# Performance work log

Hardware: AMD Instinct MI355X
Metric: run time of the kernel (lower is better)

The kernel has to match this reference:

```python
import jax, jax.numpy as jnp
import numpy as np

N, E, DIN, DH, DOUT = 50000, 800000, 128, 256, 128
EPS = 1e-5
SLOPE = 0.01  # torch leaky_relu default


def setup_inputs() -> dict:
    key = jax.random.key(0)
    ks = jax.random.split(key, 8)
    w = lambda k, shape: jax.random.normal(k, shape, jnp.float32) * 0.05
    return {
        "x": jax.random.normal(ks[0], (N, DIN), jnp.float32),
        "edge_index": jax.random.randint(ks[1], (2, E), 0, N, jnp.int32),
        "W0": w(ks[2], (DH, DIN)),  "b0": jnp.zeros((DH,), jnp.float32),
        "g0": jnp.ones((DH,), jnp.float32), "be0": jnp.zeros((DH,), jnp.float32),
        "W1": w(ks[3], (DH, DH)),   "b1": jnp.zeros((DH,), jnp.float32),
        "g1": jnp.ones((DH,), jnp.float32), "be1": jnp.zeros((DH,), jnp.float32),
        "W2": w(ks[4], (DOUT, DH)), "b2": jnp.zeros((DOUT,), jnp.float32),
        "g2": jnp.ones((DOUT,), jnp.float32), "be2": jnp.zeros((DOUT,), jnp.float32),
    }


def _gcn_forward(x, edge_index, params):
    n = x.shape[0]
    loop = jnp.arange(n, dtype=edge_index.dtype)
    src = jnp.concatenate([edge_index[0], loop])  # add self-loops
    dst = jnp.concatenate([edge_index[1], loop])
    deg = jnp.zeros((n,), x.dtype).at[dst].add(1.0)
    dinv = jax.lax.rsqrt(deg)  # deg >= 1 due to self-loops
    enorm = (dinv[src] * dinv[dst])[:, None]  # [E+N, 1]

    def conv(h, W, b):
        h = h @ W.T  # linear first (PyG GCNConv), messages in out_dim
        msg = h[src] * enorm
        return jax.ops.segment_sum(msg, dst, num_segments=n) + b

    def bn(h, g, be):  # BatchNorm1d, training-mode batch stats (biased var)
        mu = h.mean(0)
        var = ((h - mu) ** 2).mean(0)
        return (h - mu) * jax.lax.rsqrt(var + EPS) * g + be

    (W0, b0, g0, be0, W1, b1, g1, be1, W2, b2, g2, be2) = params
    h = jax.nn.leaky_relu(bn(conv(x, W0, b0), g0, be0), SLOPE)
    h = jax.nn.leaky_relu(bn(conv(h, W1, b1), g1, be1), SLOPE)
    h = bn(conv(h, W2, b2), g2, be2)  # last layer: no leaky_relu
    return h


def reference(x, edge_index, W0, b0, g0, be0, W1, b1, g1, be1, W2, b2, g2, be2):
    return _gcn_forward(x, edge_index,
                        (W0, b0, g0, be0, W1, b1, g1, be1, W2, b2, g2, be2))
```

## Files before the change

### kernel.cpp

```cpp
#include <hip/hip_runtime.h>
#include <hip/hip_bf16.h>

#define N_NODES 50000
#define N_EDGES 800000
#define DIN 128
#define DH   256
#define DOUT 128
#define EPSV 1e-5f
#define SLOPE 0.01f
#define SCAN_NB ((N_NODES + 255) / 256)

typedef __bf16 bf16x8 __attribute__((ext_vector_type(8)));
typedef __bf16 bf16x4 __attribute__((ext_vector_type(4)));
typedef float  f32x4  __attribute__((ext_vector_type(4)));

__global__ void cast_kernel(const float* __restrict__ src, __bf16* __restrict__ dst, int n4) {
    int i = blockIdx.x * blockDim.x + threadIdx.x;
    if (i < n4) {
        float4 v = ((const float4*)src)[i];
        bf16x4 o; o[0] = (__bf16)v.x; o[1] = (__bf16)v.y; o[2] = (__bf16)v.z; o[3] = (__bf16)v.w;
        ((bf16x4*)dst)[i] = o;
    }
}

__global__ void deg_kernel(const int* __restrict__ dst, int* __restrict__ deg) {
    int i = blockIdx.x * blockDim.x + threadIdx.x;
    if (i < N_EDGES) atomicAdd(&deg[dst[i]], 1);
}

__global__ void dinv_kernel(const int* __restrict__ deg, float* __restrict__ dinv) {
    int i = blockIdx.x * blockDim.x + threadIdx.x;
    if (i < N_NODES) dinv[i] = rsqrtf((float)deg[i] + 1.0f);
}

__global__ __launch_bounds__(256) void scan_bsum(const int* __restrict__ deg,
                                                 int* __restrict__ bsum) {
    __shared__ int lds[256];
    int i = blockIdx.x * 256 + threadIdx.x;
    lds[threadIdx.x] = (i < N_NODES) ? deg[i] + 1 : 0;
    __syncthreads();
    #pragma unroll
    for (int off = 128; off > 0; off >>= 1) {
        if (threadIdx.x < off) lds[threadIdx.x] += lds[threadIdx.x + off];
        __syncthreads();
    }
    if (threadIdx.x == 0) bsum[blockIdx.x] = lds[0];
}

__global__ __launch_bounds__(256) void scan_boffs(const int* __restrict__ bsum,
                                                  int* __restrict__ boffs) {
    __shared__ int lds[256];
    const int t = threadIdx.x;
    lds[t] = (t < SCAN_NB) ? bsum[t] : 0;
    __syncthreads();
    #pragma unroll
    for (int off = 1; off < 256; off <<= 1) {
        int add = (t >= off) ? lds[t - off] : 0;
        __syncthreads();
        lds[t] += add;
        __syncthreads();
    }
    boffs[t] = (t == 0) ? 0 : lds[t - 1];
}

__global__ __launch_bounds__(256) void scan_write(const int* __restrict__ deg,
                                                  const int* __restrict__ boffs,
                                                  int* __restrict__ rp) {
    __shared__ int lds[256];
    const int t = threadIdx.x;
    int i = blockIdx.x * 256 + t;
    int v = (i < N_NODES) ? deg[i] + 1 : 0;
    lds[t] = v;
    __syncthreads();
    #pragma unroll
    for (int off = 1; off < 256; off <<= 1) {
        int add = (t >= off) ? lds[t - off] : 0;
        __syncthreads();
        lds[t] += add;
        __syncthreads();
    }
    if (i < N_NODES) rp[i] = boffs[blockIdx.x] + lds[t] - v;
    if (i == N_NODES - 1) rp[N_NODES] = boffs[blockIdx.x] + lds[t];
}

__global__ void scatter_kernel(const int* __restrict__ ei, const float* __restrict__ dinv,
                               const int* __restrict__ rp, int* __restrict__ cursor,
                               int2* __restrict__ csr) {
    int e = blockIdx.x * blockDim.x + threadIdx.x;
    if (e >= N_EDGES + N_NODES) return;
    int pos, src; float w;
    if (e < N_EDGES) {
        src = ei[e]; int dst = ei[N_EDGES + e];
        w = dinv[src] * dinv[dst];
        pos = rp[dst] + atomicAdd(&cursor[dst], 1);
    } else {
        src = e - N_EDGES;
        w = dinv[src] * dinv[src];
        pos = rp[src + 1] - 1;
    }
    csr[pos] = make_int2(src, __float_as_int(w));
}

template<int C8, bool OUTF32>
__global__ __launch_bounds__(256) void spmm_b(const int* __restrict__ rp,
                                              const int2* __restrict__ csr,
                                              const __bf16* __restrict__ h,
                                              void* __restrict__ outp) {
    constexpr int C = C8 * 8;
    constexpr int RPB = 256 / C8;
    const int r = blockIdx.x * RPB + threadIdx.x / C8;
    const int l = threadIdx.x % C8;
    if (r >= N_NODES) return;
    const bf16x8* __restrict__ h8 = (const bf16x8*)h;
    const int e0 = rp[r], e1 = rp[r + 1];
    float acc0[8] = {}, acc1[8] = {};
    int e = e0;
    for (; e + 8 <= e1; e += 8) {
        int2 p[8];
        #pragma unroll
        for (int u = 0; u < 8; ++u) p[u] = csr[e + u];
        bf16x8 v[8];
        #pragma unroll
        for (int u = 0; u < 8; ++u) v[u] = h8[(long)p[u].x * C8 + l];
        #pragma unroll
        for (int u = 0; u < 8; ++u) {
            float w = __int_as_float(p[u].y);
            #pragma unroll
            for (int j = 0; j < 8; ++j) {
                if (u & 1) acc1[j] = fmaf(w, (float)v[u][j], acc1[j]);
                else       acc0[j] = fmaf(w, (float)v[u][j], acc0[j]);
            }
        }
    }
    for (; e + 2 <= e1; e += 2) {
        int2 p0 = csr[e], p1 = csr[e + 1];
        float w0 = __int_as_float(p0.y), w1 = __int_as_float(p1.y);
        bf16x8 v0 = h8[(long)p0.x * C8 + l];
        bf16x8 v1 = h8[(long)p1.x * C8 + l];
        #pragma unroll
        for (int j = 0; j < 8; ++j) {
            acc0[j] = fmaf(w0, (float)v0[j], acc0[j]);
            acc1[j] = fmaf(w1, (float)v1[j], acc1[j]);
        }
    }
    if (e < e1) {
        int2 p0 = csr[e];
        float w0 = __int_as_float(p0.y);
        bf16x8 v0 = h8[(long)p0.x * C8 + l];
        #pragma unroll
        for (int j = 0; j < 8; ++j) acc0[j] = fmaf(w0, (float)v0[j], acc0[j]);
    }
    float res[8];
    #pragma unroll
    for (int j = 0; j < 8; ++j) res[j] = acc0[j] + acc1[j];
    if (OUTF32) {
        float* o = (float*)outp + (long)r * C + l * 8;
        ((float4*)o)[0] = make_float4(res[0], res[1], res[2], res[3]);
        ((float4*)o)[1] = make_float4(res[4], res[5], res[6], res[7]);
    } else {
        bf16x8 ob;
        #pragma unroll
        for (int j = 0; j < 8; ++j) ob[j] = (__bf16)res[j];
        ((bf16x8*)outp)[(long)r * C8 + l] = ob;
    }
}

template<int K, int NC, bool FUSE_BN, bool RELU>
__global__ __launch_bounds__(256) void gemm_tile(const __bf16* __restrict__ A,
                                                 const __bf16* __restrict__ W,
                                                 const float* __restrict__ ss,
                                                 __bf16* __restrict__ C,
                                                 int M) {
    constexpr int NW = NC / 64;
    constexpr int MW = 4 / NW;
    constexpr int BM = MW * 64;
    constexpr int LSTR = 40;
    __shared__ __bf16 As[BM][LSTR];

    const int tid = threadIdx.x;
    const int wave = tid >> 6, lane = tid & 63;
    const int ln15 = lane & 15, kg = lane >> 4;
    const int wm = wave / NW, wn = wave % NW;
    const int m0 = blockIdx.x * BM;

    const int srow = tid >> 2;
    const int schunk = tid & 3;

    f32x4 acc[4][4];
    #pragma unroll
    for (int i = 0; i < 4; ++i)
        #pragma unroll
        for (int j = 0; j < 4; ++j) acc[i][j] = (f32x4){0.f, 0.f, 0.f, 0.f};

    for (int kt = 0; kt < K; kt += 32) {
        #pragma unroll
        for (int p = 0; p < MW; ++p) {
            int gr = m0 + p * 64 + srow;
            gr = gr < M ? gr : M - 1;
            bf16x8 v = *(const bf16x8*)(A + (long)gr * K + kt + schunk * 8);
            if (FUSE_BN) {
                const f32x4* ss4 = (const f32x4*)ss;
                int ci = (kt + schunk * 8) >> 2;
                f32x4 sc0 = ss4[ci],            sc1 = ss4[ci + 1];
                f32x4 sh0 = ss4[(K >> 2) + ci], sh1 = ss4[(K >> 2) + ci + 1];
                float f[8];
                #pragma unroll
                for (int j = 0; j < 4; ++j) {
                    f[j]     = fmaf((float)v[j],     sc0[j], sh0[j]);
                    f[j + 4] = fmaf((float)v[j + 4], sc1[j], sh1[j]);
                }
                if (RELU) {
                    #pragma unroll
                    for (int j = 0; j < 8; ++j) f[j] = f[j] > 0.f ? f[j] : SLOPE * f[j];
                }
                #pragma unroll
                for (int j = 0; j < 8; ++j) v[j] = (__bf16)f[j];
            }
            *(bf16x8*)(&As[p * 64 + srow][schunk * 8]) = v;
        }
        __syncthreads();
        bf16x8 b[4];
        #pragma unroll
        for (int j = 0; j < 4; ++j)
            b[j] = *(const bf16x8*)(W + (long)(wn * 64 + j * 16 + ln15) * K + kt + kg * 8);
        #pragma unroll
        for (int i = 0; i < 4; ++i) {
            bf16x8 a = *(const bf16x8*)(&As[wm * 64 + i * 16 + ln15][kg * 8]);
            #pragma unroll
            for (int j = 0; j < 4; ++j)
                acc[i][j] = __builtin_amdgcn_mfma_f32_16x16x32_bf16(a, b[j], acc[i][j], 0, 0, 0);
        }
        __syncthreads();
    }
    #pragma unroll
    for (int i = 0; i < 4; ++i) {
        #pragma unroll
        for (int j = 0; j < 4; ++j) {
            #pragma unroll
            for (int q = 0; q < 4; ++q) {
                int r = m0 + wm * 64 + i * 16 + kg * 4 + q;
                if (r < M) C[(long)r * NC + wn * 64 + j * 16 + ln15] = (__bf16)acc[i][j][q];
            }
        }
    }
}

#define NB_STATS 128
template<int C, bool BF16>
__global__ __launch_bounds__(256) void bn_stats(const void* __restrict__ hp,
                                                float* __restrict__ partial) {
    constexpr int LPR = C / 4;
    constexpr int RPI = 256 / LPR;
    const int chunk = threadIdx.x % LPR;
    const int rof   = threadIdx.x / LPR;
    float s[4] = {}, s2[4] = {};
    for (int r = blockIdx.x * RPI + rof; r < N_NODES; r += NB_STATS * RPI) {
        float v[4];
        if (BF16) {
            bf16x4 x = ((const bf16x4*)hp)[(long)r * LPR + chunk];
            #pragma unroll
            for (int j = 0; j < 4; ++j) v[j] = (float)x[j];
        } else {
            float4 x = ((const float4*)hp)[(long)r * LPR + chunk];
            v[0] = x.x; v[1] = x.y; v[2] = x.z; v[3] = x.w;
        }
        #pragma unroll
        for (int j = 0; j < 4; ++j) { s[j] += v[j]; s2[j] += v[j] * v[j]; }
    }
    __shared__ float red[256 * 8];
    #pragma unroll
    for (int j = 0; j < 4; ++j) { red[threadIdx.x * 8 + j] = s[j]; red[threadIdx.x * 8 + 4 + j] = s2[j]; }
    __syncthreads();
    if (rof == 0) {
        #pragma unroll
        for (int g = 1; g < RPI; ++g) {
            #pragma unroll
            for (int j = 0; j < 4; ++j) {
                s[j]  += red[(g * LPR + chunk) * 8 + j];
                s2[j] += red[(g * LPR + chunk) * 8 + 4 + j];
            }
        }
        #pragma unroll
        for (int j = 0; j < 4; ++j) {
            partial[blockIdx.x * 2 * C + chunk * 4 + j]     = s[j];
            partial[blockIdx.x * 2 * C + C + chunk * 4 + j] = s2[j];
        }
    }
}

template<int C>
__global__ void bn_reduce(const float* __restrict__ partial, const float* __restrict__ g,
                          const float* __restrict__ be, float* __restrict__ ss) {
    int c = threadIdx.x;
    float s_0 = 0.f, s_1 = 0.f, q_0 = 0.f, q_1 = 0.f;
    #pragma unroll 4
    for (int b = 0; b < NB_STATS; b += 2) {
        s_0 += partial[b * 2 * C + c];
        q_0 += partial[b * 2 * C + C + c];
        s_1 += partial[(b + 1) * 2 * C + c];
        q_1 += partial[(b + 1) * 2 * C + C + c];
    }
    float s = s_0 + s_1, s2 = q_0 + q_1;
    const float invn = 1.0f / (float)N_NODES;
    float mean = s * invn;
    float var  = s2 * invn - mean * mean;
    float rstd = rsqrtf(var + EPSV);
    float sc = g[c] * rstd;
    ss[c] = sc;
    ss[C + c] = be[c] - mean * sc;
}

template<int C>
__global__ __launch_bounds__(256) void bn_apply_f32(float* __restrict__ h,
                                                    const float* __restrict__ ss) {
    constexpr int LPR = C / 4;
    const long total = (long)N_NODES * LPR;
    const long stride = (long)gridDim.x * blockDim.x;
    for (long idx = (long)blockIdx.x * blockDim.x + threadIdx.x; idx < total; idx += stride) {
        int chunk = (int)(idx % LPR);
        float4 sc = ((const float4*)ss)[chunk];
        float4 sh = ((const float4*)(ss + C))[chunk];
        float4 x = ((float4*)h)[idx];
        x.x = fmaf(x.x, sc.x, sh.x); x.y = fmaf(x.y, sc.y, sh.y);
        x.z = fmaf(x.z, sc.z, sh.z); x.w = fmaf(x.w, sc.w, sh.w);
        ((float4*)h)[idx] = x;
    }
}

extern "C" void kernel_launch(void* const* d_in, const int* in_sizes, int n_in,
                              void* d_out, int out_size, void* d_ws, size_t ws_size,
                              hipStream_t stream) {
    const float* x   = (const float*)d_in[0];
    const int*   ei  = (const int*)  d_in[1];
    const float* W0  = (const float*)d_in[2];
    const float* g0  = (const float*)d_in[4];
    const float* be0 = (const float*)d_in[5];
    const float* W1  = (const float*)d_in[6];
    const float* g1  = (const float*)d_in[8];
    const float* be1 = (const float*)d_in[9];
    const float* W2  = (const float*)d_in[10];
    const float* g2  = (const float*)d_in[12];
    const float* be2 = (const float*)d_in[13];
    float* out = (float*)d_out;

    char* wsb = (char*)d_ws;
    auto alloc = [&](size_t bytes) { char* p = wsb; wsb += (bytes + 255) & ~255UL; return p; };
    int*    deg     = (int*)   alloc(N_NODES * 4);
    int*    rp      = (int*)   alloc((N_NODES + 4) * 4);
    int*    cursor  = (int*)   alloc(N_NODES * 4);
    float*  dinv    = (float*) alloc(N_NODES * 4);
    int*    bsum    = (int*)   alloc(256 * 4);
    int*    boffs   = (int*)   alloc(257 * 4);
    float*  partial = (float*) alloc(NB_STATS * 2 * DH * 4);
    float*  ss      = (float*) alloc(2 * DH * 4);
    int2*   csr     = (int2*)  alloc((size_t)(N_EDGES + N_NODES) * 8);
    __bf16* w0b     = (__bf16*)alloc(DH * DIN * 2);
    __bf16* w1b     = (__bf16*)alloc(DH * DH * 2);
    __bf16* w2b     = (__bf16*)alloc(DOUT * DH * 2);
    __bf16* xb      = (__bf16*)alloc((size_t)N_NODES * DIN * 2);
    __bf16* bf0     = (__bf16*)alloc((size_t)N_NODES * DH * 2);
    __bf16* bf1     = (__bf16*)alloc((size_t)N_NODES * DH * 2);

    cast_kernel<<<(DH * DIN / 4 + 255) / 256, 256, 0, stream>>>(W0, w0b, DH * DIN / 4);
    cast_kernel<<<(DH * DH  / 4 + 255) / 256, 256, 0, stream>>>(W1, w1b, DH * DH / 4);
    cast_kernel<<<(DOUT * DH / 4 + 255) / 256, 256, 0, stream>>>(W2, w2b, DOUT * DH / 4);
    cast_kernel<<<(N_NODES * DIN / 4 + 255) / 256, 256, 0, stream>>>(x, xb, N_NODES * DIN / 4);

    hipMemsetAsync(deg, 0, N_NODES * 4, stream);
    hipMemsetAsync(cursor, 0, N_NODES * 4, stream);
    deg_kernel<<<(N_EDGES + 255) / 256, 256, 0, stream>>>(ei + N_EDGES, deg);
    dinv_kernel<<<(N_NODES + 255) / 256, 256, 0, stream>>>(deg, dinv);
    scan_bsum<<<SCAN_NB, 256, 0, stream>>>(deg, bsum);
    scan_boffs<<<1, 256, 0, stream>>>(bsum, boffs);
    scan_write<<<SCAN_NB, 256, 0, stream>>>(deg, boffs, rp);
    scatter_kernel<<<(N_EDGES + N_NODES + 255) / 256, 256, 0, stream>>>(
        ei, dinv, rp, cursor, csr);

    spmm_b<DIN / 8, false><<<(N_NODES * (DIN / 8) + 255) / 256, 256, 0, stream>>>(
        rp, csr, xb, bf0);
    gemm_tile<DIN, DH, false, false><<<(N_NODES + 63) / 64, 256, 0, stream>>>(
        bf0, w0b, nullptr, bf1, N_NODES);
    bn_stats<DH, true><<<NB_STATS, 256, 0, stream>>>(bf1, partial);
    bn_reduce<DH><<<1, DH, 0, stream>>>(partial, g0, be0, ss);

    gemm_tile<DH, DH, true, true><<<(N_NODES + 63) / 64, 256, 0, stream>>>(
        bf1, w1b, ss, bf0, N_NODES);
    spmm_b<DH / 8, false><<<(N_NODES * (DH / 8) + 255) / 256, 256, 0, stream>>>(
        rp, csr, bf0, bf1);
    bn_stats<DH, true><<<NB_STATS, 256, 0, stream>>>(bf1, partial);
    bn_reduce<DH><<<1, DH, 0, stream>>>(partial, g1, be1, ss);

    gemm_tile<DH, DOUT, true, true><<<(N_NODES + 127) / 128, 256, 0, stream>>>(
        bf1, w2b, ss, bf0, N_NODES);
    spmm_b<DOUT / 8, true><<<(N_NODES * (DOUT / 8) + 255) / 256, 256, 0, stream>>>(
        rp, csr, bf0, out);
    bn_stats<DOUT, false><<<NB_STATS, 256, 0, stream>>>(out, partial);
    bn_reduce<DOUT><<<1, DOUT, 0, stream>>>(partial, g2, be2, ss);
    bn_apply_f32<DOUT><<<2048, 256, 0, stream>>>(out, ss);
}
```

Before: 403.8 us.

## Factor symmetric normalization out of SpMM and double-buffer GEMM A tiles

The per-edge weight dinv[src]*dinv[dst] is split into a row pre-scale by dinv[src] and a post-scale by dinv[dst]. The pre-scale is folded into the x cast and into the GEMM epilogue, and the post-scale is applied once per output row in the SpMM. This halves the CSR entry size to one int per edge and drops the per-edge weight multiply. The GEMM A-tile loading is also rewritten with double-buffered LDS and register prefetch, so the next tile's loads overlap the MFMA work at the cost of more LDS and registers.

```diff
diff --git a/kernel.cpp b/kernel.cpp
--- a/kernel.cpp
+++ b/kernel.cpp
@@ -20,6 +20,23 @@
         float4 v = ((const float4*)src)[i];
         bf16x4 o; o[0] = (__bf16)v.x; o[1] = (__bf16)v.y; o[2] = (__bf16)v.z; o[3] = (__bf16)v.w;
         ((bf16x4*)dst)[i] = o;
+    }
+}
+
+__global__ void cast_scale_kernel(const float* __restrict__ src, const float* __restrict__ dinv,
+                                  __bf16* __restrict__ dst) {
+    int i = blockIdx.x * blockDim.x + threadIdx.x;
+    if (i < N_NODES * DIN / 8) {
+        int row = i / (DIN / 8);
+        float d = dinv[row];
+        float4 a = ((const float4*)src)[i * 2];
+        float4 b = ((const float4*)src)[i * 2 + 1];
+        bf16x8 o;
+        o[0] = (__bf16)(a.x * d); o[1] = (__bf16)(a.y * d);
+        o[2] = (__bf16)(a.z * d); o[3] = (__bf16)(a.w * d);
+        o[4] = (__bf16)(b.x * d); o[5] = (__bf16)(b.y * d);
+        o[6] = (__bf16)(b.z * d); o[7] = (__bf16)(b.w * d);
+        ((bf16x8*)dst)[i] = o;
     }
 }
 
@@ -83,27 +100,26 @@
     if (i == N_NODES - 1) rp[N_NODES] = boffs[blockIdx.x] + lds[t];
 }
 
-__global__ void scatter_kernel(const int* __restrict__ ei, const float* __restrict__ dinv,
+__global__ void scatter_kernel(const int* __restrict__ ei,
                                const int* __restrict__ rp, int* __restrict__ cursor,
-                               int2* __restrict__ csr) {
+                               int* __restrict__ csr) {
     int e = blockIdx.x * blockDim.x + threadIdx.x;
     if (e >= N_EDGES + N_NODES) return;
-    int pos, src; float w;
+    int pos, src;
     if (e < N_EDGES) {
         src = ei[e]; int dst = ei[N_EDGES + e];
-        w = dinv[src] * dinv[dst];
         pos = rp[dst] + atomicAdd(&cursor[dst], 1);
     } else {
         src = e - N_EDGES;
-        w = dinv[src] * dinv[src];
         pos = rp[src + 1] - 1;
     }
-    csr[pos] = make_int2(src, __float_as_int(w));
+    csr[pos] = src;
 }
 
 template<int C8, bool OUTF32>
 __global__ __launch_bounds__(256) void spmm_b(const int* __restrict__ rp,
-                                              const int2* __restrict__ csr,
+                                              const int* __restrict__ csr,
+                                              const float* __restrict__ dinv,
                                               const __bf16* __restrict__ h,
                                               void* __restrict__ outp) {
     constexpr int C = C8 * 8;
@@ -116,43 +132,41 @@
     float acc0[8] = {}, acc1[8] = {};
     int e = e0;
     for (; e + 8 <= e1; e += 8) {
-        int2 p[8];
+        int p[8];
         #pragma unroll
         for (int u = 0; u < 8; ++u) p[u] = csr[e + u];
         bf16x8 v[8];
         #pragma unroll
-        for (int u = 0; u < 8; ++u) v[u] = h8[(long)p[u].x * C8 + l];
+        for (int u = 0; u < 8; ++u) v[u] = h8[(long)p[u] * C8 + l];
         #pragma unroll
         for (int u = 0; u < 8; ++u) {
-            float w = __int_as_float(p[u].y);
             #pragma unroll
             for (int j = 0; j < 8; ++j) {
-                if (u & 1) acc1[j] = fmaf(w, (float)v[u][j], acc1[j]);
-                else       acc0[j] = fmaf(w, (float)v[u][j], acc0[j]);
+                if (u & 1) acc1[j] += (float)v[u][j];
+                else       acc0[j] += (float)v[u][j];
             }
         }
     }
     for (; e + 2 <= e1; e += 2) {
-        int2 p0 = csr[e], p1 = csr[e + 1];
-        float w0 = __int_as_float(p0.y), w1 = __int_as_float(p1.y);
-        bf16x8 v0 = h8[(long)p0.x * C8 + l];
-        bf16x8 v1 = h8[(long)p1.x * C8 + l];
+        int p0 = csr[e], p1 = csr[e + 1];
+        bf16x8 v0 = h8[(long)p0 * C8 + l];
+        bf16x8 v1 = h8[(long)p1 * C8 + l];
         #pragma unroll
         for (int j = 0; j < 8; ++j) {
-            acc0[j] = fmaf(w0, (float)v0[j], acc0[j]);
-            acc1[j] = fmaf(w1, (float)v1[j], acc1[j]);
+            acc0[j] += (float)v0[j];
+            acc1[j] += (float)v1[j];
         }
     }
     if (e < e1) {
-        int2 p0 = csr[e];
-        float w0 = __int_as_float(p0.y);
-        bf16x8 v0 = h8[(long)p0.x * C8 + l];
-        #pragma unroll
-        for (int j = 0; j < 8; ++j) acc0[j] = fmaf(w0, (float)v0[j], acc0[j]);
-    }
+        int p0 = csr[e];
+        bf16x8 v0 = h8[(long)p0 * C8 + l];
+        #pragma unroll
+        for (int j = 0; j < 8; ++j) acc0[j] += (float)v0[j];
+    }
+    const float d = dinv[r];
     float res[8];
     #pragma unroll
-    for (int j = 0; j < 8; ++j) res[j] = acc0[j] + acc1[j];
+    for (int j = 0; j < 8; ++j) res[j] = (acc0[j] + acc1[j]) * d;
     if (OUTF32) {
         float* o = (float*)outp + (long)r * C + l * 8;
         ((float4*)o)[0] = make_float4(res[0], res[1], res[2], res[3]);
@@ -165,26 +179,32 @@
     }
 }
 
-template<int K, int NC, bool FUSE_BN, bool RELU>
+template<int K, int NC, bool FUSE_BN, bool RELU, bool SCALE>
 __global__ __launch_bounds__(256) void gemm_tile(const __bf16* __restrict__ A,
                                                  const __bf16* __restrict__ W,
                                                  const float* __restrict__ ss,
+                                                 const float* __restrict__ dinv,
                                                  __bf16* __restrict__ C,
                                                  int M) {
     constexpr int NW = NC / 64;
     constexpr int MW = 4 / NW;
     constexpr int BM = MW * 64;
-    constexpr int LSTR = 40;
-    __shared__ __bf16 As[BM][LSTR];
+    constexpr int NSTEP = K / 32;
+    __shared__ __bf16 As[2][BM][40];
 
     const int tid = threadIdx.x;
     const int wave = tid >> 6, lane = tid & 63;
     const int ln15 = lane & 15, kg = lane >> 4;
     const int wm = wave / NW, wn = wave % NW;
     const int m0 = blockIdx.x * BM;
-
-    const int srow = tid >> 2;
-    const int schunk = tid & 3;
+    const int srow = tid >> 2, schunk = tid & 3;
+
+    int grow[MW];
+    #pragma unroll
+    for (int p = 0; p < MW; ++p) {
+        int gr = m0 + p * 64 + srow;
+        grow[p] = gr < M ? gr : M - 1;
+    }
 
     f32x4 acc[4][4];
     #pragma unroll
@@ -192,54 +212,93 @@
         #pragma unroll
         for (int j = 0; j < 4; ++j) acc[i][j] = (f32x4){0.f, 0.f, 0.f, 0.f};
 
-    for (int kt = 0; kt < K; kt += 32) {
-        #pragma unroll
-        for (int p = 0; p < MW; ++p) {
-            int gr = m0 + p * 64 + srow;
-            gr = gr < M ? gr : M - 1;
-            bf16x8 v = *(const bf16x8*)(A + (long)gr * K + kt + schunk * 8);
-            if (FUSE_BN) {
-                const f32x4* ss4 = (const f32x4*)ss;
-                int ci = (kt + schunk * 8) >> 2;
-                f32x4 sc0 = ss4[ci],            sc1 = ss4[ci + 1];
-                f32x4 sh0 = ss4[(K >> 2) + ci], sh1 = ss4[(K >> 2) + ci + 1];
-                float f[8];
-                #pragma unroll
-                for (int j = 0; j < 4; ++j) {
-                    f[j]     = fmaf((float)v[j],     sc0[j], sh0[j]);
-                    f[j + 4] = fmaf((float)v[j + 4], sc1[j], sh1[j]);
-                }
-                if (RELU) {
-                    #pragma unroll
-                    for (int j = 0; j < 8; ++j) f[j] = f[j] > 0.f ? f[j] : SLOPE * f[j];
-                }
-                #pragma unroll
-                for (int j = 0; j < 8; ++j) v[j] = (__bf16)f[j];
-            }
-            *(bf16x8*)(&As[p * 64 + srow][schunk * 8]) = v;
-        }
-        __syncthreads();
+#define LOAD_A(vv, kt_)                                                         \
+    _Pragma("unroll")                                                           \
+    for (int p = 0; p < MW; ++p)                                                \
+        vv[p] = *(const bf16x8*)(A + (long)grow[p] * K + (kt_) + schunk * 8);
+
+#define XFORM_A(vv, kt_)                                                        \
+    if (FUSE_BN) {                                                              \
+        const f32x4* ss4 = (const f32x4*)ss;                                    \
+        int ci = ((kt_) + schunk * 8) >> 2;                                     \
+        f32x4 sc0 = ss4[ci],            sc1 = ss4[ci + 1];                      \
+        f32x4 sh0 = ss4[(K >> 2) + ci], sh1 = ss4[(K >> 2) + ci + 1];           \
+        _Pragma("unroll")                                                       \
+        for (int p = 0; p < MW; ++p) {                                          \
+            float f[8];                                                         \
+            _Pragma("unroll")                                                   \
+            for (int j = 0; j < 4; ++j) {                                       \
+                f[j]     = fmaf((float)vv[p][j],     sc0[j], sh0[j]);           \
+                f[j + 4] = fmaf((float)vv[p][j + 4], sc1[j], sh1[j]);           \
+            }                                                                   \
+            if (RELU) {                                                         \
+                _Pragma("unroll")                                               \
+                for (int j = 0; j < 8; ++j) f[j] = f[j] > 0.f ? f[j] : SLOPE * f[j]; \
+            }                                                                   \
+            _Pragma("unroll")                                                   \
+            for (int j = 0; j < 8; ++j) vv[p][j] = (__bf16)f[j];                \
+        }                                                                       \
+    }
+
+#define WRITE_A(buf, vv)                                                        \
+    _Pragma("unroll")                                                           \
+    for (int p = 0; p < MW; ++p)                                                \
+        *(bf16x8*)(&As[buf][p * 64 + srow][schunk * 8]) = vv[p];
+
+    bf16x8 v0[MW], v[MW];
+    LOAD_A(v0, 0)
+    XFORM_A(v0, 0)
+    WRITE_A(0, v0)
+    if (NSTEP > 1) {
+        LOAD_A(v, 32)
+        XFORM_A(v, 32)
+    }
+    __syncthreads();
+
+    int cur = 0;
+    #pragma unroll
+    for (int step = 0; step < NSTEP; ++step) {
+        const int kt = step * 32;
+        if (step + 1 < NSTEP) {
+            WRITE_A(cur ^ 1, v)
+        }
+        bf16x8 vn[MW];
+        if (step + 2 < NSTEP) {
+            LOAD_A(vn, kt + 64)
+        }
         bf16x8 b[4];
         #pragma unroll
         for (int j = 0; j < 4; ++j)
             b[j] = *(const bf16x8*)(W + (long)(wn * 64 + j * 16 + ln15) * K + kt + kg * 8);
         #pragma unroll
         for (int i = 0; i < 4; ++i) {
-            bf16x8 a = *(const bf16x8*)(&As[wm * 64 + i * 16 + ln15][kg * 8]);
+            bf16x8 a = *(const bf16x8*)(&As[cur][wm * 64 + i * 16 + ln15][kg * 8]);
             #pragma unroll
             for (int j = 0; j < 4; ++j)
                 acc[i][j] = __builtin_amdgcn_mfma_f32_16x16x32_bf16(a, b[j], acc[i][j], 0, 0, 0);
         }
-        __syncthreads();
-    }
+        if (step + 2 < NSTEP) {
+            XFORM_A(vn, kt + 64)
+            #pragma unroll
+            for (int p = 0; p < MW; ++p) v[p] = vn[p];
+        }
+        __syncthreads();
+        cur ^= 1;
+    }
+#undef LOAD_A
+#undef XFORM_A
+#undef WRITE_A
+
     #pragma unroll
     for (int i = 0; i < 4; ++i) {
         #pragma unroll
-        for (int j = 0; j < 4; ++j) {
-            #pragma unroll
-            for (int q = 0; q < 4; ++q) {
-                int r = m0 + wm * 64 + i * 16 + kg * 4 + q;
-                if (r < M) C[(long)r * NC + wn * 64 + j * 16 + ln15] = (__bf16)acc[i][j][q];
+        for (int q = 0; q < 4; ++q) {
+            int r = m0 + wm * 64 + i * 16 + kg * 4 + q;
+            if (r < M) {
+                float d = SCALE ? dinv[r] : 1.0f;
+                #pragma unroll
+                for (int j = 0; j < 4; ++j)
+                    C[(long)r * NC + wn * 64 + j * 16 + ln15] = (__bf16)(acc[i][j][q] * d);
             }
         }
     }
@@ -353,7 +412,7 @@
     int*    boffs   = (int*)   alloc(257 * 4);
     float*  partial = (float*) alloc(NB_STATS * 2 * DH * 4);
     float*  ss      = (float*) alloc(2 * DH * 4);
-    int2*   csr     = (int2*)  alloc((size_t)(N_EDGES + N_NODES) * 8);
+    int*    csr     = (int*)   alloc((size_t)(N_EDGES + N_NODES) * 4);
     __bf16* w0b     = (__bf16*)alloc(DH * DIN * 2);
     __bf16* w1b     = (__bf16*)alloc(DH * DH * 2);
     __bf16* w2b     = (__bf16*)alloc(DOUT * DH * 2);
@@ -364,7 +423,6 @@
     cast_kernel<<<(DH * DIN / 4 + 255) / 256, 256, 0, stream>>>(W0, w0b, DH * DIN / 4);
     cast_kernel<<<(DH * DH  / 4 + 255) / 256, 256, 0, stream>>>(W1, w1b, DH * DH / 4);
     cast_kernel<<<(DOUT * DH / 4 + 255) / 256, 256, 0, stream>>>(W2, w2b, DOUT * DH / 4);
-    cast_kernel<<<(N_NODES * DIN / 4 + 255) / 256, 256, 0, stream>>>(x, xb, N_NODES * DIN / 4);
 
     hipMemsetAsync(deg, 0, N_NODES * 4, stream);
     hipMemsetAsync(cursor, 0, N_NODES * 4, stream);
@@ -373,27 +431,28 @@
     scan_bsum<<<SCAN_NB, 256, 0, stream>>>(deg, bsum);
     scan_boffs<<<1, 256, 0, stream>>>(bsum, boffs);
     scan_write<<<SCAN_NB, 256, 0, stream>>>(deg, boffs, rp);
-    scatter_kernel<<<(N_EDGES + N_NODES + 255) / 256, 256, 0, stream>>>(
-        ei, dinv, rp, cursor, csr);
+    scatter_kernel<<<(N_EDGES + N_NODES + 255) / 256, 256, 0, stream>>>(ei, rp, cursor, csr);
+
+    cast_scale_kernel<<<(N_NODES * (DIN / 8) + 255) / 256, 256, 0, stream>>>(x, dinv, xb);
 
     spmm_b<DIN / 8, false><<<(N_NODES * (DIN / 8) + 255) / 256, 256, 0, stream>>>(
-        rp, csr, xb, bf0);
-    gemm_tile<DIN, DH, false, false><<<(N_NODES + 63) / 64, 256, 0, stream>>>(
-        bf0, w0b, nullptr, bf1, N_NODES);
+        rp, csr, dinv, xb, bf0);
+    gemm_tile<DIN, DH, false, false, false><<<(N_NODES + 63) / 64, 256, 0, stream>>>(
+        bf0, w0b, nullptr, nullptr, bf1, N_NODES);
     bn_stats<DH, true><<<NB_STATS, 256, 0, stream>>>(bf1, partial);
     bn_reduce<DH><<<1, DH, 0, stream>>>(partial, g0, be0, ss);
 
-    gemm_tile<DH, DH, true, true><<<(N_NODES + 63) / 64, 256, 0, stream>>>(
-        bf1, w1b, ss, bf0, N_NODES);
+    gemm_tile<DH, DH, true, true, true><<<(N_NODES + 63) / 64, 256, 0, stream>>>(
+        bf1, w1b, ss, dinv, bf0, N_NODES);
     spmm_b<DH / 8, false><<<(N_NODES * (DH / 8) + 255) / 256, 256, 0, stream>>>(
-        rp, csr, bf0, bf1);
+        rp, csr, dinv, bf0, bf1);
     bn_stats<DH, true><<<NB_STATS, 256, 0, stream>>>(bf1, partial);
     bn_reduce<DH><<<1, DH, 0, stream>>>(partial, g1, be1, ss);
 
-    gemm_tile<DH, DOUT, true, true><<<(N_NODES + 127) / 128, 256, 0, stream>>>(
-        bf1, w2b, ss, bf0, N_NODES);
+    gemm_tile<DH, DOUT, true, true, true><<<(N_NODES + 127) / 128, 256, 0, stream>>>(
+        bf1, w2b, ss, dinv, bf0, N_NODES);
     spmm_b<DOUT / 8, true><<<(N_NODES * (DOUT / 8) + 255) / 256, 256, 0, stream>>>(
-        rp, csr, bf0, out);
+        rp, csr, dinv, bf0, out);
     bn_stats<DOUT, false><<<NB_STATS, 256, 0, stream>>>(out, partial);
     bn_reduce<DOUT><<<1, DOUT, 0, stream>>>(partial, g2, be2, ss);
     bn_apply_f32<DOUT><<<2048, 256, 0, stream>>>(out, ss);
```

Result: no change. 400.0 us (-0.9%).
